# Kernel optimization log

Hardware: AMD Instinct MI355X
Metric: run time of the kernel (lower is better)

Reference implementation:

```python
import jax, jax.numpy as jnp
import numpy as np

N, L, D, H = 4, 2048, 512, 8
DK = D // H


def setup_inputs() -> dict:
    key = jax.random.key(0)
    ks = jax.random.split(key, 12)
    s = 1.0 / np.sqrt(D)
    x_q = jax.random.normal(ks[0], (N, L, D), dtype=jnp.float32)
    x_k = jax.random.normal(ks[1], (N, L, D), dtype=jnp.float32)
    x_v = jax.random.normal(ks[2], (N, L, D), dtype=jnp.float32)
    # causal attention mask (1 = keep)
    attention_mask = jnp.tril(jnp.ones((L, L), dtype=jnp.int32))
    # padding mask: random valid lengths in [L//2, L], 1 = keep
    lengths = jax.random.randint(ks[3], (N,), L // 2, L + 1)
    padding_mask = (jnp.arange(L)[None, :] < lengths[:, None]).astype(jnp.int32)
    Wq = jax.random.uniform(ks[4], (D, D), jnp.float32, -s, s)
    bq = jax.random.uniform(ks[5], (D,), jnp.float32, -s, s)
    Wk = jax.random.uniform(ks[6], (D, D), jnp.float32, -s, s)
    bk = jax.random.uniform(ks[7], (D,), jnp.float32, -s, s)
    Wv = jax.random.uniform(ks[8], (D, D), jnp.float32, -s, s)
    bv = jax.random.uniform(ks[9], (D,), jnp.float32, -s, s)
    Wo = jax.random.uniform(ks[10], (D, D), jnp.float32, -s, s)
    bo = jax.random.uniform(ks[11], (D,), jnp.float32, -s, s)
    return {"x_q": x_q, "x_k": x_k, "x_v": x_v,
            "padding_mask": padding_mask, "attention_mask": attention_mask,
            "Wq": Wq, "bq": bq, "Wk": Wk, "bk": bk,
            "Wv": Wv, "bv": bv, "Wo": Wo, "bo": bo}


def reference(x_q, x_k, x_v, padding_mask, attention_mask,
              Wq, bq, Wk, bk, Wv, bv, Wo, bo):
    n, lq, _ = x_q.shape
    lkv = x_k.shape[1]
    Q = (x_q @ Wq.T + bq).reshape(n, lq, H, DK)
    K = (x_k @ Wk.T + bk).reshape(n, lkv, H, DK)
    V = (x_v @ Wv.T + bv).reshape(n, lkv, H, DK)
    # score: [n, lq, lkv, H]
    score = jnp.einsum('nihd,njhd->nijh', Q, K) / np.sqrt(DK)
    score = jnp.where(attention_mask.reshape(1, lq, lkv, 1) == 0, -jnp.inf, score)
    score = jnp.where(padding_mask.reshape(n, 1, lkv, 1) == 0, -jnp.inf, score)
    score = jax.nn.softmax(score, axis=2)
    value = jnp.einsum('nijh,njhd->nihd', score, V).reshape(n, lq, D)
    return value @ Wo.T + bo
```

## Files before the change

### kernel.cpp

```cpp
#include <hip/hip_runtime.h>

#define NB 4
#define LSEQ 2048
#define DMODEL 512
#define NH 8
#define DKH 64

typedef __attribute__((ext_vector_type(8))) _Float16 f16x8;
typedef __attribute__((ext_vector_type(4))) float f32x4;

__device__ __forceinline__ unsigned short f2h(float f) {
  _Float16 h = (_Float16)f;
  return __builtin_bit_cast(unsigned short, h);
}

#define GLD16(gsrc, ldst)                                                     \
  __builtin_amdgcn_global_load_lds(                                           \
      (const __attribute__((address_space(1))) unsigned int*)(gsrc),          \
      (__attribute__((address_space(3))) unsigned int*)(ldst), 16, 0, 0)

__global__ __launch_bounds__(256) void prep(
    const float* __restrict__ s0, const float* __restrict__ s1,
    const float* __restrict__ s2, unsigned short* __restrict__ xh,
    const float* __restrict__ w0, const float* __restrict__ w1,
    const float* __restrict__ w2, const float* __restrict__ w3,
    unsigned short* __restrict__ wh, int nz) {
  const int bid = blockIdx.x;
  const int actBlocks = nz << 12;
  const float* src;
  unsigned short* dst;
  int i;
  if (bid < actBlocks) {
    const int z = bid >> 12;
    src = (z == 0) ? s0 : (z == 1) ? s1 : s2;
    dst = xh + (size_t)z * ((size_t)NB * LSEQ * DMODEL);
    i = ((bid & 4095) * 256 + threadIdx.x) * 4;
  } else {
    const int wb = bid - actBlocks;
    const int wi = wb >> 8;
    src = (wi == 0) ? w0 : (wi == 1) ? w1 : (wi == 2) ? w2 : w3;
    dst = wh + (size_t)wi * 262144;
    i = ((wb & 255) * 256 + threadIdx.x) * 4;
  }
  const float4 v = *(const float4*)&src[i];
  ushort4 o;
  o.x = f2h(v.x); o.y = f2h(v.y); o.z = f2h(v.z); o.w = f2h(v.w);
  *(ushort4*)&dst[i] = o;
}

template <int F16OUT>
__global__ __launch_bounds__(256, 2) void gemm1(
    const unsigned short* __restrict__ XhB, const unsigned short* __restrict__ WhB,
    const float* __restrict__ bias0, const float* __restrict__ bias1,
    const float* __restrict__ bias2, void* __restrict__ CB,
    unsigned short* __restrict__ VtOut, int zbase, int scaleq) {
  __shared__ unsigned short As[2][128 * 64];
  __shared__ unsigned short Ws[2][128 * 64];
  const size_t matE = (size_t)NB * LSEQ * DMODEL;

  const int bid = blockIdx.x;
  const int off = bid >> 3;
  const int P = (bid & 7) + 8 * (off >> 2);
  const int bx = off & 3;
  const int by = P & 63;
  const int z = P >> 6;
  const int zz = z + zbase;

  const unsigned short* Xh = XhB + (size_t)z * matE;
  const unsigned short* Wh = WhB + (size_t)z * DMODEL * DMODEL;
  const float* bias = (zz == 0) ? bias0 : (zz == 1) ? bias1 : bias2;
  const float scale = (scaleq && zz == 0) ? 0.18033688011112042f : 1.0f;
  const bool vt = F16OUT && (zz == 2);

  const int tid = threadIdx.x;
  const int w = tid >> 6, lane = tid & 63;
  const int l15 = lane & 15, l4 = lane >> 4;
  const int bn = bx * 128;
  const int bm = by * 128;
  const int wm = (w >> 1) * 64, wn = (w & 1) * 64;
  const int lr8 = lane >> 3, slot = lane & 7;

  float bi[4];
#pragma unroll
  for (int nf = 0; nf < 4; ++nf) bi[nf] = bias[bn + wn + nf * 16 + l15];

  f32x4 acc[4][4] = {};

#define STAGE_G(buf, k0)                                                      \
  {                                                                           \
    _Pragma("unroll")                                                         \
    for (int j = 0; j < 4; ++j) {                                             \
      const int seg = w * 32 + j * 8;                                         \
      const int row = seg + lr8;                                              \
      const int sc = slot ^ (row & 7);                                        \
      GLD16(Xh + (size_t)(bm + row) * DMODEL + (k0) + sc * 8,                 \
            &As[buf][seg * 64]);                                              \
      GLD16(Wh + (size_t)(bn + row) * DMODEL + (k0) + sc * 8,                 \
            &Ws[buf][seg * 64]);                                              \
    }                                                                         \
  }

  STAGE_G(0, 0);

#pragma unroll 1
  for (int it = 0; it < 8; ++it) {
    const int cur = it & 1;
    if (it < 7) {
      STAGE_G(cur ^ 1, (it + 1) * 64);
      asm volatile("s_waitcnt vmcnt(8)" ::: "memory");
    } else {
      asm volatile("s_waitcnt vmcnt(0)" ::: "memory");
    }
    __builtin_amdgcn_s_barrier();

#pragma unroll
    for (int ks = 0; ks < 2; ++ks) {
      f16x8 af[4], wf[4];
#pragma unroll
      for (int mf = 0; mf < 4; ++mf) {
        const int row = wm + mf * 16 + l15;
        const int sl = (ks * 4 + l4) ^ (row & 7);
        af[mf] = *(const f16x8*)&As[cur][row * 64 + sl * 8];
      }
#pragma unroll
      for (int nf = 0; nf < 4; ++nf) {
        const int row = wn + nf * 16 + l15;
        const int sl = (ks * 4 + l4) ^ (row & 7);
        wf[nf] = *(const f16x8*)&Ws[cur][row * 64 + sl * 8];
      }
#pragma unroll
      for (int mf = 0; mf < 4; ++mf)
#pragma unroll
        for (int nf = 0; nf < 4; ++nf)
          acc[mf][nf] = __builtin_amdgcn_mfma_f32_16x16x32_f16(af[mf], wf[nf], acc[mf][nf], 0, 0, 0);
    }
    __builtin_amdgcn_s_barrier();
  }
#undef STAGE_G

#pragma unroll
  for (int mf = 0; mf < 4; ++mf)
#pragma unroll
    for (int r = 0; r < 4; ++r) {
      const size_t row = (size_t)(bm + wm + mf * 16 + l4 * 4 + r);
#pragma unroll
      for (int nf = 0; nf < 4; ++nf) {
        const float v = (acc[mf][nf][r] + bi[nf]) * scale;
        const int col = bn + wn + nf * 16 + l15;
        if (vt) {
          const int tok = (int)row & (LSEQ - 1);
          const int nn = (int)row >> 11;
          const int hh = col >> 6, dd = col & 63;
          VtOut[((((size_t)nn * NH + hh) * DKH + dd) << 11) + tok] = f2h(v);
        } else {
          const size_t o = row * DMODEL + col;
          if (F16OUT) ((unsigned short*)CB)[z * matE + o] = f2h(v);
          else        ((float*)CB)[z * matE + o] = v;
        }
      }
    }
}

__global__ __launch_bounds__(256, 3) void flash_mfma(
    const unsigned short* __restrict__ Qb, const unsigned short* __restrict__ Kb,
    const unsigned short* __restrict__ Vt, const int* __restrict__ pad,
    unsigned short* __restrict__ OH) {
  __shared__ unsigned short Ks[2][64 * 64];
  __shared__ unsigned short Vs[2][64 * 64];
  __shared__ unsigned short Ps[64 * 64];
  __shared__ int s_nt;

  const int tid = threadIdx.x;
  const int bid = blockIdx.x;
  const int sub = bid >> 3;
  const int nh = (bid & 7) * 4 + (sub & 3);
  const int qt = 31 - (sub >> 2);
  const int n = nh >> 3, h = nh & 7;
  const int w = tid >> 6, lane = tid & 63;
  const int l15 = lane & 15, l4 = lane >> 4;
  const int lr8 = lane >> 3, slot = lane & 7;

  {
    const int v = (tid < 32) ? pad[(size_t)n * LSEQ + tid * 64] : 1;
    if (tid < 64) {
      const unsigned long long b = __ballot(v == 0);
      if (tid == 0) s_nt = b ? (int)(__ffsll(b) - 1) : 32;
    }
  }
  __syncthreads();
  const int nt = s_nt;

  int plast[4];
#pragma unroll
  for (int f = 0; f < 4; ++f)
    plast[f] = pad[(size_t)n * LSEQ + (nt - 1) * 64 + f * 16 + l15];

  f16x8 vones;
#pragma unroll
  for (int j = 0; j < 8; ++j) vones[j] = (_Float16)((l15 == 0) ? 1.0f : 0.0f);

  const size_t qrow = (size_t)(n * LSEQ + qt * 64 + w * 16 + l15) * DMODEL + h * DKH;
  const f16x8 qa0 = *(const f16x8*)(Qb + qrow + l4 * 8);
  const f16x8 qa1 = *(const f16x8*)(Qb + qrow + 32 + l4 * 8);

  f32x4 Oacc[5] = {};
  float m_[4];
#pragma unroll
  for (int r = 0; r < 4; ++r) m_[r] = -1e30f;

  const int ktend = (qt + 1 < nt) ? (qt + 1) : nt;

#pragma unroll
  for (int j = 0; j < 2; ++j) {
    const int seg = w * 16 + j * 8;
    const int row = seg + lr8;
    const int sc = slot ^ (row & 7);
    GLD16(Kb + (size_t)(n * LSEQ + row) * DMODEL + h * DKH + sc * 8, &Ks[0][seg * 64]);
    GLD16(Vt + ((size_t)nh * DKH + row) * LSEQ + sc * 8, &Vs[0][seg * 64]);
  }
  asm volatile("s_waitcnt vmcnt(0)" ::: "memory");
  __builtin_amdgcn_s_barrier();

#pragma unroll 1
  for (int kt = 0; kt < ktend; ++kt) {
    const int cur = kt & 1;
    if (kt + 1 < ktend) {
      const int nb = cur ^ 1;
#pragma unroll
      for (int j = 0; j < 2; ++j) {
        const int seg = w * 16 + j * 8;
        const int row = seg + lr8;
        const int sc = slot ^ (row & 7);
        GLD16(Kb + (size_t)(n * LSEQ + (kt + 1) * 64 + row) * DMODEL + h * DKH + sc * 8,
              &Ks[nb][seg * 64]);
        GLD16(Vt + ((size_t)nh * DKH + row) * LSEQ + (kt + 1) * 64 + sc * 8,
              &Vs[nb][seg * 64]);
      }
    }

    f32x4 S[4] = {};
#pragma unroll
    for (int f = 0; f < 4; ++f) {
      const int kr = f * 16 + l15;
      const int swz = kr & 7;
      const f16x8 b0 = *(const f16x8*)&Ks[cur][kr * 64 + ((l4 ^ swz) * 8)];
      S[f] = __builtin_amdgcn_mfma_f32_16x16x32_f16(qa0, b0, S[f], 0, 0, 0);
      const f16x8 b1 = *(const f16x8*)&Ks[cur][kr * 64 + (((4 + l4) ^ swz) * 8)];
      S[f] = __builtin_amdgcn_mfma_f32_16x16x32_f16(qa1, b1, S[f], 0, 0, 0);
    }

    if (kt == nt - 1) {
#pragma unroll
      for (int f = 0; f < 4; ++f)
        if (!plast[f]) {
#pragma unroll
          for (int r = 0; r < 4; ++r) S[f][r] = -1e30f;
        }
    }
    if (kt == qt) {
#pragma unroll
      for (int f = 0; f < 4; ++f) {
        const int col = f * 16 + l15;
#pragma unroll
        for (int r = 0; r < 4; ++r)
          if (col > w * 16 + l4 * 4 + r) S[f][r] = -1e30f;
      }
    }

    float pmax[4];
#pragma unroll
    for (int r = 0; r < 4; ++r)
      pmax[r] = fmaxf(fmaxf(S[0][r], S[1][r]), fmaxf(S[2][r], S[3][r]));
    const bool cond = (pmax[0] <= m_[0] + 11.f) && (pmax[1] <= m_[1] + 11.f) &&
                      (pmax[2] <= m_[2] + 11.f) && (pmax[3] <= m_[3] + 11.f);
    if (!__all(cond)) {
#pragma unroll
      for (int r = 0; r < 4; ++r) {
        float mx = pmax[r];
        mx = fmaxf(mx, __shfl_xor(mx, 1, 64));
        mx = fmaxf(mx, __shfl_xor(mx, 2, 64));
        mx = fmaxf(mx, __shfl_xor(mx, 4, 64));
        mx = fmaxf(mx, __shfl_xor(mx, 8, 64));
        const float mnew = fmaxf(m_[r], mx);
        const float alpha = exp2f(m_[r] - mnew);
        m_[r] = mnew;
#pragma unroll
        for (int f = 0; f < 5; ++f) Oacc[f][r] *= alpha;
      }
    }

#pragma unroll
    for (int r = 0; r < 4; ++r) {
      const int prow = w * 16 + l4 * 4 + r;
      const int psw = prow & 7;
#pragma unroll
      for (int f = 0; f < 4; ++f) {
        const float p = exp2f(S[f][r] - m_[r]);
        const int c16 = 2 * f + (l15 >> 3);
        Ps[prow * 64 + ((c16 ^ psw) * 8) + (lane & 7)] = f2h(p);
      }
    }

#pragma unroll
    for (int ks = 0; ks < 2; ++ks) {
      const int prow = w * 16 + l15;
      const f16x8 pa = *(const f16x8*)&Ps[prow * 64 + (((ks * 4 + l4) ^ (prow & 7)) * 8)];
      Oacc[4] = __builtin_amdgcn_mfma_f32_16x16x32_f16(pa, vones, Oacc[4], 0, 0, 0);
#pragma unroll
      for (int f = 0; f < 4; ++f) {
        const int vr = f * 16 + l15;
        const f16x8 vb = *(const f16x8*)&Vs[cur][vr * 64 + (((ks * 4 + l4) ^ (vr & 7)) * 8)];
        Oacc[f] = __builtin_amdgcn_mfma_f32_16x16x32_f16(pa, vb, Oacc[f], 0, 0, 0);
      }
    }

    asm volatile("s_waitcnt vmcnt(0)" ::: "memory");
    __builtin_amdgcn_s_barrier();
  }

#pragma unroll
  for (int r = 0; r < 4; ++r) {
    const float lr = __shfl(Oacc[4][r], l4 << 4, 64);
    const float inv = 1.0f / lr;
    const size_t orow = (size_t)(n * LSEQ + qt * 64 + w * 16 + l4 * 4 + r) * DMODEL + h * DKH;
#pragma unroll
    for (int f = 0; f < 4; ++f)
      OH[orow + f * 16 + l15] = f2h(Oacc[f][r] * inv);
  }
}

extern "C" void kernel_launch(void* const* d_in, const int* in_sizes, int n_in,
                              void* d_out, int out_size, void* d_ws, size_t ws_size,
                              hipStream_t stream) {
  const float* x_q = (const float*)d_in[0];
  const float* x_k = (const float*)d_in[1];
  const float* x_v = (const float*)d_in[2];
  const int*   pad = (const int*)d_in[3];
  const float* Wq = (const float*)d_in[5];  const float* bq = (const float*)d_in[6];
  const float* Wk = (const float*)d_in[7];  const float* bk = (const float*)d_in[8];
  const float* Wv = (const float*)d_in[9];  const float* bv = (const float*)d_in[10];
  const float* Wo = (const float*)d_in[11]; const float* bo = (const float*)d_in[12];
  float* out = (float*)d_out;

  const size_t matE = (size_t)NB * LSEQ * DMODEL;
  const size_t wE = (size_t)DMODEL * DMODEL;
  unsigned short* base = (unsigned short*)d_ws;
  const size_t needB = (size_t)(6 * matE + 4 * wE) * 2;
  const bool batched = ws_size >= needB;

  if (batched) {
    unsigned short* Xh  = base;
    unsigned short* Wh4 = base + 3 * matE;
    unsigned short* QKV = Wh4 + 4 * wE;
    unsigned short* Vt  = QKV + 2 * matE;
    unsigned short* OH  = base;

    prep<<<13312, 256, 0, stream>>>(x_q, x_k, x_v, Xh, Wq, Wk, Wv, Wo, Wh4, 3);
    gemm1<1><<<768, 256, 0, stream>>>(Xh, Wh4, bq, bk, bv, (void*)QKV, Vt, 0, 1);
    flash_mfma<<<1024, 256, 0, stream>>>(QKV, QKV + matE, Vt, pad, OH);
    gemm1<0><<<256, 256, 0, stream>>>(OH, Wh4 + 3 * wE, bo, bo, bo,
                                      (void*)out, nullptr, 0, 0);
  } else {
    unsigned short* Xh  = base;
    unsigned short* Wh4 = base + matE;
    unsigned short* QKV = Wh4 + 4 * wE;
    unsigned short* Vt  = QKV + 2 * matE;
    unsigned short* OH  = base;

    const float* xs[3] = {x_q, x_k, x_v};
    const float* bs[3] = {bq, bk, bv};
    for (int z = 0; z < 3; ++z) {
      prep<<<(z == 0) ? 5120 : 4096, 256, 0, stream>>>(
          xs[z], xs[z], xs[z], Xh, Wq, Wk, Wv, Wo, Wh4, 1);
      gemm1<1><<<256, 256, 0, stream>>>(Xh, Wh4 + z * wE, bs[z], bs[z], bs[z],
                                        (void*)(QKV + z * matE), Vt, z, 1);
    }
    flash_mfma<<<1024, 256, 0, stream>>>(QKV, QKV + matE, Vt, pad, OH);
    gemm1<0><<<256, 256, 0, stream>>>(OH, Wh4 + 3 * wE, bo, bo, bo,
                                      (void*)out, nullptr, 0, 0);
  }
}
```

Before: 200.7 us.

## Process 128 query rows per flash block and use narrower tiles in output GEMM

```diff
diff --git a/kernel.cpp b/kernel.cpp
--- a/kernel.cpp
+++ b/kernel.cpp
@@ -48,22 +48,27 @@
   *(ushort4*)&dst[i] = o;
 }
 
-template <int F16OUT>
-__global__ __launch_bounds__(256, 2) void gemm1(
+template <int F16OUT, int BN>
+__global__ __launch_bounds__(256, 3) void gemm1(
     const unsigned short* __restrict__ XhB, const unsigned short* __restrict__ WhB,
     const float* __restrict__ bias0, const float* __restrict__ bias1,
     const float* __restrict__ bias2, void* __restrict__ CB,
     unsigned short* __restrict__ VtOut, int zbase, int scaleq) {
+  constexpr int NF = BN / 32;
   __shared__ unsigned short As[2][128 * 64];
-  __shared__ unsigned short Ws[2][128 * 64];
+  __shared__ unsigned short Ws[2][BN * 64];
   const size_t matE = (size_t)NB * LSEQ * DMODEL;
 
   const int bid = blockIdx.x;
-  const int off = bid >> 3;
-  const int P = (bid & 7) + 8 * (off >> 2);
-  const int bx = off & 3;
-  const int by = P & 63;
-  const int z = P >> 6;
+  int bx, by, z;
+  if (BN == 128) {
+    const int off = bid >> 3;
+    const int P = (bid & 7) + 8 * (off >> 2);
+    bx = off & 3; by = P & 63; z = P >> 6;
+  } else {
+    const int i = bid >> 3;
+    by = (bid & 7) * 8 + (i & 7); bx = i >> 3; z = 0;
+  }
   const int zz = z + zbase;
 
   const unsigned short* Xh = XhB + (size_t)z * matE;
@@ -75,16 +80,16 @@
   const int tid = threadIdx.x;
   const int w = tid >> 6, lane = tid & 63;
   const int l15 = lane & 15, l4 = lane >> 4;
-  const int bn = bx * 128;
+  const int bn = bx * BN;
   const int bm = by * 128;
-  const int wm = (w >> 1) * 64, wn = (w & 1) * 64;
+  const int wm = (w >> 1) * 64, wn = (w & 1) * (NF * 16);
   const int lr8 = lane >> 3, slot = lane & 7;
 
-  float bi[4];
-#pragma unroll
-  for (int nf = 0; nf < 4; ++nf) bi[nf] = bias[bn + wn + nf * 16 + l15];
-
-  f32x4 acc[4][4] = {};
+  float bi[NF];
+#pragma unroll
+  for (int nf = 0; nf < NF; ++nf) bi[nf] = bias[bn + wn + nf * 16 + l15];
+
+  f32x4 acc[4][NF] = {};
 
 #define STAGE_G(buf, k0)                                                      \
   {                                                                           \
@@ -95,6 +100,12 @@
       const int sc = slot ^ (row & 7);                                        \
       GLD16(Xh + (size_t)(bm + row) * DMODEL + (k0) + sc * 8,                 \
             &As[buf][seg * 64]);                                              \
+    }                                                                         \
+    _Pragma("unroll")                                                         \
+    for (int j = 0; j < NF; ++j) {                                            \
+      const int seg = w * (NF * 8) + j * 8;                                   \
+      const int row = seg + lr8;                                              \
+      const int sc = slot ^ (row & 7);                                        \
       GLD16(Wh + (size_t)(bn + row) * DMODEL + (k0) + sc * 8,                 \
             &Ws[buf][seg * 64]);                                              \
     }                                                                         \
@@ -107,7 +118,11 @@
     const int cur = it & 1;
     if (it < 7) {
       STAGE_G(cur ^ 1, (it + 1) * 64);
-      asm volatile("s_waitcnt vmcnt(8)" ::: "memory");
+      if (BN == 128) {
+        asm volatile("s_waitcnt vmcnt(8)" ::: "memory");
+      } else {
+        asm volatile("s_waitcnt vmcnt(6)" ::: "memory");
+      }
     } else {
       asm volatile("s_waitcnt vmcnt(0)" ::: "memory");
     }
@@ -115,7 +130,7 @@
 
 #pragma unroll
     for (int ks = 0; ks < 2; ++ks) {
-      f16x8 af[4], wf[4];
+      f16x8 af[4], wf[NF];
 #pragma unroll
       for (int mf = 0; mf < 4; ++mf) {
         const int row = wm + mf * 16 + l15;
@@ -123,7 +138,7 @@
         af[mf] = *(const f16x8*)&As[cur][row * 64 + sl * 8];
       }
 #pragma unroll
-      for (int nf = 0; nf < 4; ++nf) {
+      for (int nf = 0; nf < NF; ++nf) {
         const int row = wn + nf * 16 + l15;
         const int sl = (ks * 4 + l4) ^ (row & 7);
         wf[nf] = *(const f16x8*)&Ws[cur][row * 64 + sl * 8];
@@ -131,7 +146,7 @@
 #pragma unroll
       for (int mf = 0; mf < 4; ++mf)
 #pragma unroll
-        for (int nf = 0; nf < 4; ++nf)
+        for (int nf = 0; nf < NF; ++nf)
           acc[mf][nf] = __builtin_amdgcn_mfma_f32_16x16x32_f16(af[mf], wf[nf], acc[mf][nf], 0, 0, 0);
     }
     __builtin_amdgcn_s_barrier();
@@ -144,7 +159,7 @@
     for (int r = 0; r < 4; ++r) {
       const size_t row = (size_t)(bm + wm + mf * 16 + l4 * 4 + r);
 #pragma unroll
-      for (int nf = 0; nf < 4; ++nf) {
+      for (int nf = 0; nf < NF; ++nf) {
         const float v = (acc[mf][nf][r] + bi[nf]) * scale;
         const int col = bn + wn + nf * 16 + l15;
         if (vt) {
@@ -167,14 +182,14 @@
     unsigned short* __restrict__ OH) {
   __shared__ unsigned short Ks[2][64 * 64];
   __shared__ unsigned short Vs[2][64 * 64];
-  __shared__ unsigned short Ps[64 * 64];
+  __shared__ unsigned short Ps[128 * 64];
   __shared__ int s_nt;
 
   const int tid = threadIdx.x;
   const int bid = blockIdx.x;
   const int sub = bid >> 3;
   const int nh = (bid & 7) * 4 + (sub & 3);
-  const int qt = 31 - (sub >> 2);
+  const int qt = 15 - (sub >> 2);
   const int n = nh >> 3, h = nh & 7;
   const int w = tid >> 6, lane = tid & 63;
   const int l15 = lane & 15, l4 = lane >> 4;
@@ -199,16 +214,24 @@
 #pragma unroll
   for (int j = 0; j < 8; ++j) vones[j] = (_Float16)((l15 == 0) ? 1.0f : 0.0f);
 
-  const size_t qrow = (size_t)(n * LSEQ + qt * 64 + w * 16 + l15) * DMODEL + h * DKH;
-  const f16x8 qa0 = *(const f16x8*)(Qb + qrow + l4 * 8);
-  const f16x8 qa1 = *(const f16x8*)(Qb + qrow + 32 + l4 * 8);
-
-  f32x4 Oacc[5] = {};
-  float m_[4];
-#pragma unroll
-  for (int r = 0; r < 4; ++r) m_[r] = -1e30f;
-
-  const int ktend = (qt + 1 < nt) ? (qt + 1) : nt;
+  const size_t qbase = (size_t)(n * LSEQ + qt * 128 + w * 32) * DMODEL + h * DKH;
+  f16x8 qa[2][2];
+#pragma unroll
+  for (int qh = 0; qh < 2; ++qh) {
+    const size_t qrow = qbase + (size_t)(qh * 16 + l15) * DMODEL;
+    qa[qh][0] = *(const f16x8*)(Qb + qrow + l4 * 8);
+    qa[qh][1] = *(const f16x8*)(Qb + qrow + 32 + l4 * 8);
+  }
+
+  f32x4 Oacc[2][5] = {};
+  float m_[2][4];
+#pragma unroll
+  for (int qh = 0; qh < 2; ++qh)
+#pragma unroll
+    for (int r = 0; r < 4; ++r) m_[qh][r] = -1e30f;
+
+  const int kcap = 2 * qt + 2;
+  const int ktend = (kcap < nt) ? kcap : nt;
 
 #pragma unroll
   for (int j = 0; j < 2; ++j) {
@@ -238,15 +261,18 @@
       }
     }
 
-    f32x4 S[4] = {};
+    f32x4 S[2][4] = {};
 #pragma unroll
     for (int f = 0; f < 4; ++f) {
       const int kr = f * 16 + l15;
       const int swz = kr & 7;
       const f16x8 b0 = *(const f16x8*)&Ks[cur][kr * 64 + ((l4 ^ swz) * 8)];
-      S[f] = __builtin_amdgcn_mfma_f32_16x16x32_f16(qa0, b0, S[f], 0, 0, 0);
       const f16x8 b1 = *(const f16x8*)&Ks[cur][kr * 64 + (((4 + l4) ^ swz) * 8)];
-      S[f] = __builtin_amdgcn_mfma_f32_16x16x32_f16(qa1, b1, S[f], 0, 0, 0);
+#pragma unroll
+      for (int qh = 0; qh < 2; ++qh) {
+        S[qh][f] = __builtin_amdgcn_mfma_f32_16x16x32_f16(qa[qh][0], b0, S[qh][f], 0, 0, 0);
+        S[qh][f] = __builtin_amdgcn_mfma_f32_16x16x32_f16(qa[qh][1], b1, S[qh][f], 0, 0, 0);
+      }
     }
 
     if (kt == nt - 1) {
@@ -254,63 +280,83 @@
       for (int f = 0; f < 4; ++f)
         if (!plast[f]) {
 #pragma unroll
-          for (int r = 0; r < 4; ++r) S[f][r] = -1e30f;
+          for (int qh = 0; qh < 2; ++qh)
+#pragma unroll
+            for (int r = 0; r < 4; ++r) S[qh][f][r] = -1e30f;
         }
     }
-    if (kt == qt) {
+    if (kt >= 2 * qt) {
 #pragma unroll
       for (int f = 0; f < 4; ++f) {
-        const int col = f * 16 + l15;
-#pragma unroll
-        for (int r = 0; r < 4; ++r)
-          if (col > w * 16 + l4 * 4 + r) S[f][r] = -1e30f;
-      }
-    }
-
-    float pmax[4];
-#pragma unroll
-    for (int r = 0; r < 4; ++r)
-      pmax[r] = fmaxf(fmaxf(S[0][r], S[1][r]), fmaxf(S[2][r], S[3][r]));
-    const bool cond = (pmax[0] <= m_[0] + 11.f) && (pmax[1] <= m_[1] + 11.f) &&
-                      (pmax[2] <= m_[2] + 11.f) && (pmax[3] <= m_[3] + 11.f);
+        const int gcol = kt * 64 + f * 16 + l15;
+#pragma unroll
+        for (int qh = 0; qh < 2; ++qh)
+#pragma unroll
+          for (int r = 0; r < 4; ++r) {
+            const int grow = qt * 128 + w * 32 + qh * 16 + l4 * 4 + r;
+            if (gcol > grow) S[qh][f][r] = -1e30f;
+          }
+      }
+    }
+
+    float pmax[2][4];
+    bool cond = true;
+#pragma unroll
+    for (int qh = 0; qh < 2; ++qh)
+#pragma unroll
+      for (int r = 0; r < 4; ++r) {
+        pmax[qh][r] = fmaxf(fmaxf(S[qh][0][r], S[qh][1][r]),
+                            fmaxf(S[qh][2][r], S[qh][3][r]));
+        cond = cond && (pmax[qh][r] <= m_[qh][r] + 11.f);
+      }
     if (!__all(cond)) {
 #pragma unroll
+      for (int qh = 0; qh < 2; ++qh)
+#pragma unroll
+        for (int r = 0; r < 4; ++r) {
+          float mx = pmax[qh][r];
+          mx = fmaxf(mx, __shfl_xor(mx, 1, 64));
+          mx = fmaxf(mx, __shfl_xor(mx, 2, 64));
+          mx = fmaxf(mx, __shfl_xor(mx, 4, 64));
+          mx = fmaxf(mx, __shfl_xor(mx, 8, 64));
+          const float mnew = fmaxf(m_[qh][r], mx);
+          const float alpha = exp2f(m_[qh][r] - mnew);
+          m_[qh][r] = mnew;
+#pragma unroll
+          for (int f = 0; f < 5; ++f) Oacc[qh][f][r] *= alpha;
+        }
+    }
+
+#pragma unroll
+    for (int qh = 0; qh < 2; ++qh)
+#pragma unroll
       for (int r = 0; r < 4; ++r) {
-        float mx = pmax[r];
-        mx = fmaxf(mx, __shfl_xor(mx, 1, 64));
-        mx = fmaxf(mx, __shfl_xor(mx, 2, 64));
-        mx = fmaxf(mx, __shfl_xor(mx, 4, 64));
-        mx = fmaxf(mx, __shfl_xor(mx, 8, 64));
-        const float mnew = fmaxf(m_[r], mx);
-        const float alpha = exp2f(m_[r] - mnew);
-        m_[r] = mnew;
-#pragma unroll
-        for (int f = 0; f < 5; ++f) Oacc[f][r] *= alpha;
-      }
-    }
-
-#pragma unroll
-    for (int r = 0; r < 4; ++r) {
-      const int prow = w * 16 + l4 * 4 + r;
-      const int psw = prow & 7;
-#pragma unroll
-      for (int f = 0; f < 4; ++f) {
-        const float p = exp2f(S[f][r] - m_[r]);
-        const int c16 = 2 * f + (l15 >> 3);
-        Ps[prow * 64 + ((c16 ^ psw) * 8) + (lane & 7)] = f2h(p);
-      }
-    }
+        const int prow = w * 32 + qh * 16 + l4 * 4 + r;
+        const int psw = prow & 7;
+#pragma unroll
+        for (int f = 0; f < 4; ++f) {
+          const float p = exp2f(S[qh][f][r] - m_[qh][r]);
+          const int c16 = 2 * f + (l15 >> 3);
+          Ps[prow * 64 + ((c16 ^ psw) * 8) + (lane & 7)] = f2h(p);
+        }
+      }
 
 #pragma unroll
     for (int ks = 0; ks < 2; ++ks) {
-      const int prow = w * 16 + l15;
-      const f16x8 pa = *(const f16x8*)&Ps[prow * 64 + (((ks * 4 + l4) ^ (prow & 7)) * 8)];
-      Oacc[4] = __builtin_amdgcn_mfma_f32_16x16x32_f16(pa, vones, Oacc[4], 0, 0, 0);
+      f16x8 pa[2];
+#pragma unroll
+      for (int qh = 0; qh < 2; ++qh) {
+        const int prow = w * 32 + qh * 16 + l15;
+        pa[qh] = *(const f16x8*)&Ps[prow * 64 + (((ks * 4 + l4) ^ (prow & 7)) * 8)];
+        Oacc[qh][4] = __builtin_amdgcn_mfma_f32_16x16x32_f16(pa[qh], vones, Oacc[qh][4], 0, 0, 0);
+      }
 #pragma unroll
       for (int f = 0; f < 4; ++f) {
         const int vr = f * 16 + l15;
         const f16x8 vb = *(const f16x8*)&Vs[cur][vr * 64 + (((ks * 4 + l4) ^ (vr & 7)) * 8)];
-        Oacc[f] = __builtin_amdgcn_mfma_f32_16x16x32_f16(pa, vb, Oacc[f], 0, 0, 0);
+#pragma unroll
+        for (int qh = 0; qh < 2; ++qh)
+          Oacc[qh][f] = __builtin_amdgcn_mfma_f32_16x16x32_f16(pa[qh], vb, Oacc[qh][f], 0, 0, 0);
       }
     }
 
@@ -319,14 +365,17 @@
   }
 
 #pragma unroll
-  for (int r = 0; r < 4; ++r) {
-    const float lr = __shfl(Oacc[4][r], l4 << 4, 64);
-    const float inv = 1.0f / lr;
-    const size_t orow = (size_t)(n * LSEQ + qt * 64 + w * 16 + l4 * 4 + r) * DMODEL + h * DKH;
-#pragma unroll
-    for (int f = 0; f < 4; ++f)
-      OH[orow + f * 16 + l15] = f2h(Oacc[f][r] * inv);
-  }
+  for (int qh = 0; qh < 2; ++qh)
+#pragma unroll
+    for (int r = 0; r < 4; ++r) {
+      const float lr = __shfl(Oacc[qh][4][r], l4 << 4, 64);
+      const float inv = 1.0f / lr;
+      const size_t orow =
+          (size_t)(n * LSEQ + qt * 128 + w * 32 + qh * 16 + l4 * 4 + r) * DMODEL + h * DKH;
+#pragma unroll
+      for (int f = 0; f < 4; ++f)
+        OH[orow + f * 16 + l15] = f2h(Oacc[qh][f][r] * inv);
+    }
 }
 
 extern "C" void kernel_launch(void* const* d_in, const int* in_sizes, int n_in,
@@ -356,10 +405,10 @@
     unsigned short* OH  = base;
 
     prep<<<13312, 256, 0, stream>>>(x_q, x_k, x_v, Xh, Wq, Wk, Wv, Wo, Wh4, 3);
-    gemm1<1><<<768, 256, 0, stream>>>(Xh, Wh4, bq, bk, bv, (void*)QKV, Vt, 0, 1);
-    flash_mfma<<<1024, 256, 0, stream>>>(QKV, QKV + matE, Vt, pad, OH);
-    gemm1<0><<<256, 256, 0, stream>>>(OH, Wh4 + 3 * wE, bo, bo, bo,
-                                      (void*)out, nullptr, 0, 0);
+    gemm1<1, 128><<<768, 256, 0, stream>>>(Xh, Wh4, bq, bk, bv, (void*)QKV, Vt, 0, 1);
+    flash_mfma<<<512, 256, 0, stream>>>(QKV, QKV + matE, Vt, pad, OH);
+    gemm1<0, 64><<<512, 256, 0, stream>>>(OH, Wh4 + 3 * wE, bo, bo, bo,
+                                          (void*)out, nullptr, 0, 0);
   } else {
     unsigned short* Xh  = base;
     unsigned short* Wh4 = base + matE;
@@ -372,11 +421,11 @@
     for (int z = 0; z < 3; ++z) {
       prep<<<(z == 0) ? 5120 : 4096, 256, 0, stream>>>(
           xs[z], xs[z], xs[z], Xh, Wq, Wk, Wv, Wo, Wh4, 1);
-      gemm1<1><<<256, 256, 0, stream>>>(Xh, Wh4 + z * wE, bs[z], bs[z], bs[z],
-                                        (void*)(QKV + z * matE), Vt, z, 1);
-    }
-    flash_mfma<<<1024, 256, 0, stream>>>(QKV, QKV + matE, Vt, pad, OH);
-    gemm1<0><<<256, 256, 0, stream>>>(OH, Wh4 + 3 * wE, bo, bo, bo,
-                                      (void*)out, nullptr, 0, 0);
+      gemm1<1, 128><<<256, 256, 0, stream>>>(Xh, Wh4 + z * wE, bs[z], bs[z], bs[z],
+                                             (void*)(QKV + z * matE), Vt, z, 1);
+    }
+    flash_mfma<<<512, 256, 0, stream>>>(QKV, QKV + matE, Vt, pad, OH);
+    gemm1<0, 64><<<512, 256, 0, stream>>>(OH, Wh4 + 3 * wE, bo, bo, bo,
+                                          (void*)out, nullptr, 0, 0);
   }
 }
```

New measurement: 217.5 us. 1.08x slower.
